# Performance work log

Hardware: AMD Instinct MI355X
Metric: run time of the kernel (lower is better)

Reference implementation:

```python
import jax, jax.numpy as jnp
import numpy as np

# Model dims (match init_kwargs)
B, S = 2, 2048
H = 1024          # hidden_size
I = 256           # intermediate_size
E = 256           # n_routed_experts
K = 8             # num_experts_per_tok
G = 8             # n_group
TG = 4            # topk_group
NS = 2            # n_shared_experts


def setup_inputs() -> dict:
    key = jax.random.key(0)
    ks = jax.random.split(key, 6)
    s = 0.02
    return {
        "x": jax.random.normal(ks[0], (B, S, H), jnp.float32),
        "Wg": jax.random.normal(ks[1], (E, H), jnp.float32) * s,          # gate Linear weight [E,H] (y = x @ Wg.T)
        "W_gate_up": jax.random.normal(ks[2], (E, H, 2 * I), jnp.float32) * s,  # per-expert gate_up proj
        "W_down": jax.random.normal(ks[3], (E, I, H), jnp.float32) * s,          # per-expert down proj
        "Ws_gate_up": jax.random.normal(ks[4], (NS, H, 2 * I), jnp.float32) * s, # shared experts
        "Ws_down": jax.random.normal(ks[5], (NS, I, H), jnp.float32) * s,
    }


def _mlp(x, w_gu, w_d):
    # DeepSeekV3 MLP: down( silu(gate) * up ); gate/up are the two chunks of gate_up
    gu = x @ w_gu                      # [N, 2I]
    g, u = gu[..., :I], gu[..., I:]
    return (jax.nn.silu(g) * u) @ w_d  # [N, H]


def reference(x, Wg, W_gate_up, W_down, Ws_gate_up, Ws_down):
    b, s, h = x.shape
    xf = x.reshape(-1, h)              # [N, H]
    n = xf.shape[0]

    # ---- shared experts (always active, averaged) ----
    shared = (_mlp(xf, Ws_gate_up[0], Ws_down[0]) + _mlp(xf, Ws_gate_up[1], Ws_down[1])) / NS

    # ---- grouped top-k gating ----
    logits = xf @ Wg.T                               # [N, E]
    gsize = E // G
    gl = logits.reshape(n, G, gsize)                 # [N, G, gsize]
    g_top_l, g_top_i = jax.lax.top_k(gl, TG)         # top-TG within each group
    cand_l = g_top_l.reshape(n, G * TG)              # candidate logits (group-major)
    cand_i = g_top_i.reshape(n, G * TG)              # within-group expert ids
    top_l, pos = jax.lax.top_k(cand_l, K)            # global top-K over candidates
    topk_idx = (pos // TG) * gsize + jnp.take_along_axis(cand_i, pos, axis=1)  # [N, K]
    topk_w = jax.nn.softmax(top_l, axis=-1)          # [N, K]

    # ---- routed experts: sort-by-expert + grouped GEMM (ragged_dot) ----
    flat_idx = topk_idx.reshape(-1)                  # [N*K]
    flat_w = topk_w.reshape(-1)
    order = jnp.argsort(flat_idx)                    # tokens grouped by expert id
    tok = order // K                                 # source token of each assignment
    xs = xf[tok]                                     # [N*K, H] gathered tokens, expert-contiguous
    gsz = jnp.bincount(flat_idx, length=E).astype(jnp.int32)  # tokens per expert

    gu = jax.lax.ragged_dot(xs, W_gate_up, gsz)      # [N*K, 2I] grouped GEMM 1
    hmid = jax.nn.silu(gu[:, :I]) * gu[:, I:]
    yo = jax.lax.ragged_dot(hmid, W_down, gsz)       # [N*K, H] grouped GEMM 2
    yo = yo * flat_w[order][:, None]                 # weight by gate prob

    routed = jnp.zeros_like(xf).at[tok].add(yo)      # scatter-add combine

    return (shared + routed).reshape(b, s, h)
```

## Files before the change

kernel.cpp:

```cpp
#include <hip/hip_runtime.h>
#include <hip/hip_bf16.h>


typedef __attribute__((ext_vector_type(4))) float  f32x4;
typedef __attribute__((ext_vector_type(8))) short  bf16x8;
typedef __attribute__((ext_vector_type(4))) short  bf16x4;
typedef __attribute__((ext_vector_type(4))) unsigned short u16x4;

#define DI static __device__ __forceinline__

DI unsigned short f2bf(float f){
  unsigned u = __builtin_bit_cast(unsigned, f);
  return (unsigned short)((u + 0x7FFFu + ((u>>16)&1u)) >> 16);
}
DI float bf2f(unsigned short s){
  return __builtin_bit_cast(float, ((unsigned)s)<<16);
}

#define WS_XBF      0u
#define WS_HSH      8388608u
#define WS_HMID     12582912u
#define WS_YSLOT    29360128u
#define WS_WGT      29360128u
#define WS_TOPKI    96468992u
#define WS_TOPKW    96600064u
#define WS_TOKMAP   96731136u
#define WS_SLOTMAP  96862208u
#define WS_CNT      96993280u
#define WS_CURSOR   96994304u
#define WS_ZERO     96995328u
#define WS_OFF      96999424u

__global__ __launch_bounds__(256) void k_wgT(const float* __restrict__ Wg, float* __restrict__ WgT){
  __shared__ float t[64][65];
  const int tid = threadIdx.x;
  const int hx = blockIdx.x * 64;
  const int ex = blockIdx.y * 64;
  #pragma unroll
  for (int k=0;k<16;++k){
    int i = (tid>>6)*16 + k, j = tid&63;
    t[i][j] = Wg[(size_t)(ex+i)*1024 + hx + j];
  }
  __syncthreads();
  #pragma unroll
  for (int k=0;k<16;++k){
    int i = (tid>>6)*16 + k, j = tid&63;
    WgT[(size_t)(hx+i)*256 + ex + j] = t[j][i];
  }
}

__global__ __launch_bounds__(256) void k_router(const float* __restrict__ x, const float* __restrict__ WgT,
                                                unsigned short* __restrict__ xbf,
                                                int* __restrict__ topki, float* __restrict__ topkw,
                                                int* __restrict__ cnt){
  __shared__ float xs[8][1024];
  __shared__ float lg[8][256];
  __shared__ float cv[8][32];
  __shared__ int   ce[8][32];
  const int tid = threadIdx.x;
  const int t0  = blockIdx.x * 8;
  {
    const f32x4* xg = (const f32x4*)(x + (size_t)t0*1024);
    f32x4* xs4 = (f32x4*)&xs[0][0];
    u16x4* xb4 = (u16x4*)(xbf + (size_t)t0*1024);
    #pragma unroll
    for (int i=0;i<8;++i){
      f32x4 v = xg[tid + i*256];
      xs4[tid + i*256] = v;
      u16x4 p; p[0]=f2bf(v[0]); p[1]=f2bf(v[1]); p[2]=f2bf(v[2]); p[3]=f2bf(v[3]);
      xb4[tid + i*256] = p;
    }
  }
  __syncthreads();
  {
    f32x4 a4[8];
    #pragma unroll
    for (int t=0;t<8;++t) a4[t] = (f32x4){0.f,0.f,0.f,0.f};
    const float* wc = WgT + tid;
    for (int h4=0; h4<256; ++h4){
      float w0 = wc[(size_t)(h4*4+0)*256];
      float w1 = wc[(size_t)(h4*4+1)*256];
      float w2 = wc[(size_t)(h4*4+2)*256];
      float w3 = wc[(size_t)(h4*4+3)*256];
      f32x4 wv = (f32x4){w0,w1,w2,w3};
      #pragma unroll
      for (int t=0;t<8;++t){
        f32x4 xv = *((const f32x4*)&xs[t][0] + h4);
        a4[t] += wv * xv;
      }
    }
    #pragma unroll
    for (int t=0;t<8;++t){
      double d = ((double)a4[t][0] + (double)a4[t][1]) + ((double)a4[t][2] + (double)a4[t][3]);
      lg[t][tid] = (float)d;
    }
  }
  __syncthreads();
  if (tid < 64){
    int tok = tid>>3, grp = tid&7;
    unsigned mask = 0;
    for (int j=0;j<4;++j){
      float best = -3.4e38f; int bi = 0;
      for (int i=0;i<32;++i){
        float v = lg[tok][grp*32+i];
        if (!((mask>>i)&1u) && v > best){ best=v; bi=i; }
      }
      mask |= 1u<<bi;
      cv[tok][grp*4+j] = best; ce[tok][grp*4+j] = grp*32+bi;
    }
  }
  __syncthreads();
  if (tid < 8){
    int tok = tid; unsigned mask=0;
    float vals[8]; int es[8];
    #pragma unroll
    for (int k=0;k<8;++k){
      float best=-3.4e38f; int bp=0;
      for (int p=0;p<32;++p){
        float v = cv[tok][p];
        if (!((mask>>p)&1u) && v > best){ best=v; bp=p; }
      }
      mask|=1u<<bp; vals[k]=best; es[k]=ce[tok][bp];
    }
    float m = vals[0], s=0.f, w[8];
    #pragma unroll
    for (int k=0;k<8;++k){ w[k]=expf(vals[k]-m); s+=w[k]; }
    float inv = 1.f/s;
    #pragma unroll
    for (int k=0;k<8;++k){
      int g=(t0+tok)*8+k;
      topki[g]=es[k]; topkw[g]=w[k]*inv;
      atomicAdd(&cnt[es[k]],1);
    }
  }
}

__global__ void k_scan(const int* __restrict__ cnt, int* __restrict__ off){
  __shared__ int s[256];
  int tid=threadIdx.x;
  s[tid]=cnt[tid]; __syncthreads();
  for (int d=1; d<256; d<<=1){
    int v = (tid>=d)? s[tid-d] : 0; __syncthreads();
    s[tid]+=v; __syncthreads();
  }
  off[tid+1]=s[tid]; if(tid==0) off[0]=0;
}

__global__ void k_scatter(const int* __restrict__ topki, const int* __restrict__ off,
                          int* __restrict__ cursor, int* __restrict__ tokmap, int* __restrict__ slotmap){
  int g = blockIdx.x*256 + threadIdx.x;
  int e = topki[g];
  int p = off[e] + atomicAdd(&cursor[e], 1);
  tokmap[p] = g >> 3;
  slotmap[g] = p;
}

template<int GEMM>
__global__ __launch_bounds__(512, 4) void k_gemm(
    const unsigned short* __restrict__ A1, const unsigned short* __restrict__ A2,
    const float* __restrict__ WE, const float* __restrict__ WS,
    const int* __restrict__ cnt, const int* __restrict__ off,
    const int* __restrict__ tokmap,
    unsigned short* __restrict__ O1, unsigned short* __restrict__ O2,
    float* __restrict__ OD, const unsigned short* __restrict__ zpage)
{
  __shared__ __align__(16) char smem[65536];
  const int bx = blockIdx.x, mt = blockIdx.y, nc = blockIdx.z;
  const bool sh = (bx >= 256);
  int e = bx, s = 0, M, Moff;
  if (!sh){ M = cnt[e]; Moff = mt*256; }
  else {
    int sidx = bx - 256;
    if (GEMM==1){ s = sidx>>3; Moff = (sidx&7)*512 + mt*256; }
    else        { s = 0;       Moff = sidx*1024 + mt*256; }
    M = 4096;
  }
  if (Moff >= M) return;
  const int tid=threadIdx.x, ln=tid&63, wv=tid>>6, wm=wv>>2, wn=wv&3, lrow=ln&15, lk=ln>>4;
  const int Ktot = (GEMM==1)?1024:(sh?512:256);
  const int ldB  = (GEMM==1)?512:1024;
  const float* Bp = (GEMM==1) ? (sh? WS + (size_t)s*524288 : WE + (size_t)e*524288)
                              : (sh? WS : WE + (size_t)e*262144);
  const int offe = sh? 0 : off[e];

  const char* a_src[2];
  #pragma unroll
  for (int qi=0;qi<2;++qi){
    int row  = (wv*2+qi)*16 + (ln>>2);
    int grow = Moff + row;
    const unsigned short* p;
    if (GEMM==1){
      if (!sh) p = (grow < M)? A1 + (size_t)tokmap[offe+grow]*1024 : zpage;
      else     p = A1 + (size_t)grow*1024;
    } else {
      if (!sh) p = (grow < M)? A1 + ((size_t)offe+grow)*256 : zpage;
      else     p = A2 + (size_t)grow*512;
    }
    a_src[qi] = (const char*)p + (ln&3)*16;
  }
  const char* b_src[2];
  {
    int swz = ((wv>>1)&3)<<2;
    int cg  = (ln&31) ^ swz;
    int c4  = cg*4;
    int gcol = (GEMM==1) ? ((c4<64)? nc*64 + c4 : 256 + nc*64 + (c4-64))
                         : (nc*128 + c4);
    int rbase = 4*wv + (ln>>5);
    #pragma unroll
    for (int q=0;q<2;++q)
      b_src[q] = (const char*)(Bp + (size_t)(rbase + 2*q)*ldB + gcol);
  }

  f32x4 acc[8][2] = {};

  auto stage = [&](int buf, int k0){
    #pragma unroll
    for (int qi=0;qi<2;++qi)
      __builtin_amdgcn_global_load_lds((const void*)(a_src[qi] + (size_t)k0*2),
          (void*)(smem + buf*16384 + (wv*2+qi)*1024), 16, 0, 0);
    #pragma unroll
    for (int q=0;q<2;++q)
      __builtin_amdgcn_global_load_lds((const void*)(b_src[q] + (size_t)k0*ldB*4),
          (void*)(smem + 32768 + buf*16384 + wv*2048 + q*1024), 16, 0, 0);
  };

  auto compute = [&](int buf){
    const short* as  = (const short*)(smem + buf*16384);
    const float* bs  = (const float*)(smem + 32768 + buf*16384);
    bf16x8 bv[2];
    #pragma unroll
    for (int ni=0;ni<2;++ni){
      int tc = (GEMM==1)? (ni*64 + wn*16 + lrow) : (wn*32 + ni*16 + lrow);
      int sloff = ((((tc>>2) ^ (lk<<2))<<2) | (tc&3));
      const float* colp = bs + (size_t)lk*8*128 + sloff;
      #pragma unroll
      for (int j=0;j<8;++j){
        unsigned u = __builtin_bit_cast(unsigned, colp[(size_t)j*128]);
        bv[ni][j] = (short)((u + 0x8000u) >> 16);
      }
    }
    #pragma unroll
    for (int mi=0;mi<8;++mi){
      bf16x8 af = *(const bf16x8*)(as + (wm*128+mi*16+lrow)*32 + lk*8);
      acc[mi][0] = __builtin_amdgcn_mfma_f32_16x16x32_bf16(af, bv[0], acc[mi][0], 0,0,0);
      acc[mi][1] = __builtin_amdgcn_mfma_f32_16x16x32_bf16(af, bv[1], acc[mi][1], 0,0,0);
    }
  };

  stage(0, 0);
  const int ns = Ktot>>5;
  for (int t=0;t<ns;++t){
    int b = t&1;
    if (t+1<ns){
      stage(b^1, (t+1)<<5);
      asm volatile("s_waitcnt vmcnt(4)" ::: "memory");
    } else {
      asm volatile("s_waitcnt vmcnt(0)" ::: "memory");
    }
    asm volatile("s_barrier" ::: "memory");
    compute(b);
    asm volatile("s_barrier" ::: "memory");
  }

  if (GEMM==1){
    __syncthreads();
    unsigned short* Hs = (unsigned short*)smem;
    #pragma unroll
    for (int mi=0;mi<8;++mi){
      f32x4 g = acc[mi][0], u = acc[mi][1];
      #pragma unroll
      for (int r=0;r<4;++r){
        float gg = g[r];
        float hh = (gg / (1.f + __expf(-gg))) * u[r];
        int m = wm*128 + mi*16 + lk*4 + r;
        Hs[m*72 + wn*16 + lrow] = f2bf(hh);
      }
    }
    __syncthreads();
    #pragma unroll
    for (int i=0;i<4;++i){
      int id = tid + i*512, m = id>>3, c8 = id&7;
      int grow = Moff + m;
      if (grow < M){
        unsigned short* dst = (!sh) ? O1 + ((size_t)offe + grow)*256 + nc*64 + c8*8
                                    : O2 + (size_t)grow*512 + (size_t)s*256 + nc*64 + c8*8;
        *(f32x4*)dst = *(const f32x4*)(Hs + m*72 + c8*8);
      }
    }
  } else {
    if (sh){
      #pragma unroll
      for (int mi=0;mi<8;++mi)
        #pragma unroll
        for (int ni=0;ni<2;++ni)
          #pragma unroll
          for (int r=0;r<4;++r){
            int m = Moff + wm*128 + mi*16 + lk*4 + r;
            int c = nc*128 + wn*32 + ni*16 + lrow;
            OD[(size_t)m*1024 + c] = acc[mi][ni][r]*0.5f;
          }
    } else {
      __syncthreads();
      unsigned short* Hs = (unsigned short*)smem;
      #pragma unroll
      for (int mi=0;mi<8;++mi)
        #pragma unroll
        for (int ni=0;ni<2;++ni)
          #pragma unroll
          for (int r=0;r<4;++r){
            int m = wm*128 + mi*16 + lk*4 + r;
            int c = wn*32 + ni*16 + lrow;
            Hs[m*128 + c] = f2bf(acc[mi][ni][r]);
          }
      __syncthreads();
      #pragma unroll
      for (int i=0;i<8;++i){
        int id = tid + i*512, m = id>>4, c8 = id&15;
        int grow = Moff + m;
        if (grow < M){
          unsigned short* dst = O1 + ((size_t)offe+grow)*1024 + nc*128 + c8*8;
          *(f32x4*)dst = *(const f32x4*)(Hs + m*128 + c8*8);
        }
      }
    }
  }
}

__global__ void k_final(float* __restrict__ out, const unsigned short* __restrict__ yslot,
                        const int* __restrict__ slotmap, const float* __restrict__ topkw){
  __shared__ int sp[8]; __shared__ float sw[8];
  int t = blockIdx.x, tid = threadIdx.x;
  if (tid<8){ sp[tid]=slotmap[t*8+tid]; sw[tid]=topkw[t*8+tid]; }
  __syncthreads();
  int c = tid*4;
  f32x4 o = *(f32x4*)(out + (size_t)t*1024 + c);
  #pragma unroll
  for (int k=0;k<8;++k){
    u16x4 y = *(const u16x4*)(yslot + (size_t)sp[k]*1024 + c);
    float w = sw[k];
    o[0] += w*bf2f(y[0]); o[1] += w*bf2f(y[1]); o[2] += w*bf2f(y[2]); o[3] += w*bf2f(y[3]);
  }
  *(f32x4*)(out + (size_t)t*1024 + c) = o;
}

extern "C" void kernel_launch(void* const* d_in, const int* in_sizes, int n_in,
                              void* d_out, int out_size, void* d_ws, size_t ws_size,
                              hipStream_t stream) {
  const float* x    = (const float*)d_in[0];
  const float* Wg   = (const float*)d_in[1];
  const float* Wgu  = (const float*)d_in[2];
  const float* Wd   = (const float*)d_in[3];
  const float* Wsgu = (const float*)d_in[4];
  const float* Wsd  = (const float*)d_in[5];
  float* out = (float*)d_out;

  char* W = (char*)d_ws;
  unsigned short* xbf    = (unsigned short*)(W + WS_XBF);
  unsigned short* hsh    = (unsigned short*)(W + WS_HSH);
  unsigned short* hmid   = (unsigned short*)(W + WS_HMID);
  unsigned short* yslot  = (unsigned short*)(W + WS_YSLOT);
  float* WgT     = (float*)(W + WS_WGT);
  int*   topki   = (int*)(W + WS_TOPKI);
  float* topkw   = (float*)(W + WS_TOPKW);
  int*   tokmap  = (int*)(W + WS_TOKMAP);
  int*   slotmap = (int*)(W + WS_SLOTMAP);
  int*   cnt     = (int*)(W + WS_CNT);
  int*   cursor  = (int*)(W + WS_CURSOR);
  unsigned short* zpage = (unsigned short*)(W + WS_ZERO);
  int*   off     = (int*)(W + WS_OFF);

  hipMemsetAsync((void*)cnt, 0, 1024+1024+4096, stream);

  k_wgT    <<<dim3(16,4), 256, 0, stream>>>(Wg, WgT);
  k_router <<<512, 256, 0, stream>>>(x, WgT, xbf, topki, topkw, cnt);
  k_scan   <<<1, 256, 0, stream>>>(cnt, off);
  k_scatter<<<128, 256, 0, stream>>>(topki, off, cursor, tokmap, slotmap);
  k_gemm<1><<<dim3(272,2,4), 512, 0, stream>>>(xbf, (const unsigned short*)nullptr,
        Wgu, Wsgu, cnt, off, tokmap, hmid, hsh, out, zpage);
  k_gemm<2><<<dim3(260,4,8), 512, 0, stream>>>(hmid, hsh,
        Wd, Wsd, cnt, off, tokmap, yslot, (unsigned short*)nullptr, out, zpage);
  k_final <<<4096, 256, 0, stream>>>(out, yslot, slotmap, topkw);
}
```

Before: 352.4 us.

## Stage B weights through registers as bf16 to shrink LDS footprint

```diff
diff --git a/kernel.cpp b/kernel.cpp
--- a/kernel.cpp
+++ b/kernel.cpp
@@ -164,7 +164,7 @@
     unsigned short* __restrict__ O1, unsigned short* __restrict__ O2,
     float* __restrict__ OD, const unsigned short* __restrict__ zpage)
 {
-  __shared__ __align__(16) char smem[65536];
+  __shared__ __align__(16) char smem[49152];
   const int bx = blockIdx.x, mt = blockIdx.y, nc = blockIdx.z;
   const bool sh = (bx >= 256);
   int e = bx, s = 0, M, Moff;
@@ -198,46 +198,50 @@
     }
     a_src[qi] = (const char*)p + (ln&3)*16;
   }
-  const char* b_src[2];
-  {
-    int swz = ((wv>>1)&3)<<2;
-    int cg  = (ln&31) ^ swz;
-    int c4  = cg*4;
-    int gcol = (GEMM==1) ? ((c4<64)? nc*64 + c4 : 256 + nc*64 + (c4-64))
-                         : (nc*128 + c4);
-    int rbase = 4*wv + (ln>>5);
-    #pragma unroll
-    for (int q=0;q<2;++q)
-      b_src[q] = (const char*)(Bp + (size_t)(rbase + 2*q)*ldB + gcol);
-  }
+  const int b_kk = 4*wv + (ln>>4);
+  const int b_c0 = (ln&15)*8;
+  const float* b_base[2];
+  #pragma unroll
+  for (int q=0;q<2;++q){
+    int c = b_c0 + 4*q;
+    int gcol = (GEMM==1)? ((c<64)? nc*64 + c : 256 + nc*64 + (c-64)) : (nc*128 + c);
+    b_base[q] = Bp + (size_t)b_kk*ldB + gcol;
+  }
+  const int b_wcol = b_c0 ^ ((wv>>1)<<3);
 
   f32x4 acc[8][2] = {};
-
-  auto stage = [&](int buf, int k0){
+  f32x4 brg0[2], brg1[2];
+
+  auto stageA = [&](int buf, int k0){
     #pragma unroll
     for (int qi=0;qi<2;++qi)
       __builtin_amdgcn_global_load_lds((const void*)(a_src[qi] + (size_t)k0*2),
           (void*)(smem + buf*16384 + (wv*2+qi)*1024), 16, 0, 0);
+  };
+  auto loadB = [&](f32x4* brg, int k0){
     #pragma unroll
     for (int q=0;q<2;++q)
-      __builtin_amdgcn_global_load_lds((const void*)(b_src[q] + (size_t)k0*ldB*4),
-          (void*)(smem + 32768 + buf*16384 + wv*2048 + q*1024), 16, 0, 0);
+      brg[q] = *(const f32x4*)(b_base[q] + (size_t)k0*ldB);
   };
-
+  auto writeB = [&](const f32x4* brg, int buf){
+    bf16x8 v;
+    #pragma unroll
+    for (int q=0;q<2;++q)
+      #pragma unroll
+      for (int j=0;j<4;++j)
+        v[q*4+j] = (short)f2bf(brg[q][j]);
+    *(bf16x8*)(smem + 32768 + buf*8192 + (b_kk*128 + b_wcol)*2) = v;
+  };
   auto compute = [&](int buf){
-    const short* as  = (const short*)(smem + buf*16384);
-    const float* bs  = (const float*)(smem + 32768 + buf*16384);
+    const short* as = (const short*)(smem + buf*16384);
+    const short* bs = (const short*)(smem + 32768 + buf*8192);
     bf16x8 bv[2];
     #pragma unroll
     for (int ni=0;ni<2;++ni){
       int tc = (GEMM==1)? (ni*64 + wn*16 + lrow) : (wn*32 + ni*16 + lrow);
-      int sloff = ((((tc>>2) ^ (lk<<2))<<2) | (tc&3));
-      const float* colp = bs + (size_t)lk*8*128 + sloff;
-      #pragma unroll
-      for (int j=0;j<8;++j){
-        unsigned u = __builtin_bit_cast(unsigned, colp[(size_t)j*128]);
-        bv[ni][j] = (short)((u + 0x8000u) >> 16);
-      }
+      const short* p = bs + lk*8*128 + (tc ^ (lk<<3));
+      #pragma unroll
+      for (int j=0;j<8;++j) bv[ni][j] = p[j*128];
     }
     #pragma unroll
     for (int mi=0;mi<8;++mi){
@@ -247,18 +251,33 @@
     }
   };
 
-  stage(0, 0);
   const int ns = Ktot>>5;
-  for (int t=0;t<ns;++t){
-    int b = t&1;
+  loadB(brg0, 0);
+  stageA(0, 0);
+  loadB(brg1, 32);
+  asm volatile("s_waitcnt vmcnt(2)" ::: "memory");
+  writeB(brg0, 0);
+  asm volatile("s_waitcnt lgkmcnt(0)" ::: "memory");
+  asm volatile("s_barrier" ::: "memory");
+  for (int t=0; t<ns; t+=2){
+    if (t+1<ns) stageA(1, (t+1)<<5);
+    compute(0);
     if (t+1<ns){
-      stage(b^1, (t+1)<<5);
-      asm volatile("s_waitcnt vmcnt(4)" ::: "memory");
-    } else {
       asm volatile("s_waitcnt vmcnt(0)" ::: "memory");
+      writeB(brg1, 1);
+      if (t+2<ns) loadB(brg0, (t+2)<<5);
+      asm volatile("s_waitcnt lgkmcnt(0)" ::: "memory");
     }
     asm volatile("s_barrier" ::: "memory");
-    compute(b);
+    if (t+1>=ns) break;
+    if (t+2<ns) stageA(0, (t+2)<<5);
+    compute(1);
+    if (t+2<ns){
+      asm volatile("s_waitcnt vmcnt(0)" ::: "memory");
+      writeB(brg0, 0);
+      if (t+3<ns) loadB(brg1, (t+3)<<5);
+      asm volatile("s_waitcnt lgkmcnt(0)" ::: "memory");
+    }
     asm volatile("s_barrier" ::: "memory");
   }
 
@@ -300,26 +319,31 @@
             OD[(size_t)m*1024 + c] = acc[mi][ni][r]*0.5f;
           }
     } else {
-      __syncthreads();
       unsigned short* Hs = (unsigned short*)smem;
       #pragma unroll
-      for (int mi=0;mi<8;++mi)
+      for (int pass=0; pass<2; ++pass){
+        __syncthreads();
+        if ((wn>>1) == pass){
+          #pragma unroll
+          for (int mi=0;mi<8;++mi)
+            #pragma unroll
+            for (int ni=0;ni<2;++ni)
+              #pragma unroll
+              for (int r=0;r<4;++r){
+                int m = wm*128 + mi*16 + lk*4 + r;
+                int c = (wn&1)*32 + ni*16 + lrow;
+                Hs[m*72 + c] = f2bf(acc[mi][ni][r]);
+              }
+        }
+        __syncthreads();
         #pragma unroll
-        for (int ni=0;ni<2;++ni)
-          #pragma unroll
-          for (int r=0;r<4;++r){
-            int m = wm*128 + mi*16 + lk*4 + r;
-            int c = wn*32 + ni*16 + lrow;
-            Hs[m*128 + c] = f2bf(acc[mi][ni][r]);
+        for (int i=0;i<4;++i){
+          int id = tid + i*512, m = id>>3, c8 = id&7;
+          int grow = Moff + m;
+          if (grow < M){
+            unsigned short* dst = O1 + ((size_t)offe+grow)*1024 + nc*128 + pass*64 + c8*8;
+            *(f32x4*)dst = *(const f32x4*)(Hs + m*72 + c8*8);
           }
-      __syncthreads();
-      #pragma unroll
-      for (int i=0;i<8;++i){
-        int id = tid + i*512, m = id>>4, c8 = id&15;
-        int grow = Moff + m;
-        if (grow < M){
-          unsigned short* dst = O1 + ((size_t)offe+grow)*1024 + nc*128 + c8*8;
-          *(f32x4*)dst = *(const f32x4*)(Hs + m*128 + c8*8);
         }
       }
     }
```

Result: slower. 377.2 us (+7.0%).

## Fuse weighted scatter-add combine into down-proj GEMM epilogue via atomics

Applied to the files above, without the earlier changes.

```diff
diff --git a/kernel.cpp b/kernel.cpp
--- a/kernel.cpp
+++ b/kernel.cpp
@@ -20,12 +20,11 @@
 #define WS_XBF      0u
 #define WS_HSH      8388608u
 #define WS_HMID     12582912u
-#define WS_YSLOT    29360128u
 #define WS_WGT      29360128u
 #define WS_TOPKI    96468992u
 #define WS_TOPKW    96600064u
 #define WS_TOKMAP   96731136u
-#define WS_SLOTMAP  96862208u
+#define WS_WMAP     96862208u
 #define WS_CNT      96993280u
 #define WS_CURSOR   96994304u
 #define WS_ZERO     96995328u
@@ -146,13 +145,14 @@
   off[tid+1]=s[tid]; if(tid==0) off[0]=0;
 }
 
-__global__ void k_scatter(const int* __restrict__ topki, const int* __restrict__ off,
-                          int* __restrict__ cursor, int* __restrict__ tokmap, int* __restrict__ slotmap){
+__global__ void k_scatter(const int* __restrict__ topki, const float* __restrict__ topkw,
+                          const int* __restrict__ off, int* __restrict__ cursor,
+                          int* __restrict__ tokmap, float* __restrict__ wmap){
   int g = blockIdx.x*256 + threadIdx.x;
   int e = topki[g];
   int p = off[e] + atomicAdd(&cursor[e], 1);
   tokmap[p] = g >> 3;
-  slotmap[g] = p;
+  wmap[p]   = topkw[g];
 }
 
 template<int GEMM>
@@ -160,7 +160,7 @@
     const unsigned short* __restrict__ A1, const unsigned short* __restrict__ A2,
     const float* __restrict__ WE, const float* __restrict__ WS,
     const int* __restrict__ cnt, const int* __restrict__ off,
-    const int* __restrict__ tokmap,
+    const int* __restrict__ tokmap, const float* __restrict__ wmap,
     unsigned short* __restrict__ O1, unsigned short* __restrict__ O2,
     float* __restrict__ OD, const unsigned short* __restrict__ zpage)
 {
@@ -297,50 +297,31 @@
           for (int r=0;r<4;++r){
             int m = Moff + wm*128 + mi*16 + lk*4 + r;
             int c = nc*128 + wn*32 + ni*16 + lrow;
-            OD[(size_t)m*1024 + c] = acc[mi][ni][r]*0.5f;
+            atomicAdd(&OD[(size_t)m*1024 + c], acc[mi][ni][r]*0.5f);
           }
     } else {
       __syncthreads();
-      unsigned short* Hs = (unsigned short*)smem;
+      int*   stok = (int*)smem;
+      float* swgt = (float*)(smem + 1024);
+      if (tid < 256){
+        int gr = Moff + tid;
+        if (gr < M){ stok[tid] = tokmap[offe+gr]; swgt[tid] = wmap[offe+gr]; }
+      }
+      __syncthreads();
       #pragma unroll
       for (int mi=0;mi<8;++mi)
         #pragma unroll
         for (int ni=0;ni<2;++ni)
           #pragma unroll
           for (int r=0;r<4;++r){
-            int m = wm*128 + mi*16 + lk*4 + r;
-            int c = wn*32 + ni*16 + lrow;
-            Hs[m*128 + c] = f2bf(acc[mi][ni][r]);
+            int lr = wm*128 + mi*16 + lk*4 + r;
+            if (Moff + lr < M){
+              int c = nc*128 + wn*32 + ni*16 + lrow;
+              atomicAdd(&OD[(size_t)stok[lr]*1024 + c], swgt[lr]*acc[mi][ni][r]);
+            }
           }
-      __syncthreads();
-      #pragma unroll
-      for (int i=0;i<8;++i){
-        int id = tid + i*512, m = id>>4, c8 = id&15;
-        int grow = Moff + m;
-        if (grow < M){
-          unsigned short* dst = O1 + ((size_t)offe+grow)*1024 + nc*128 + c8*8;
-          *(f32x4*)dst = *(const f32x4*)(Hs + m*128 + c8*8);
-        }
-      }
-    }
-  }
-}
-
-__global__ void k_final(float* __restrict__ out, const unsigned short* __restrict__ yslot,
-                        const int* __restrict__ slotmap, const float* __restrict__ topkw){
-  __shared__ int sp[8]; __shared__ float sw[8];
-  int t = blockIdx.x, tid = threadIdx.x;
-  if (tid<8){ sp[tid]=slotmap[t*8+tid]; sw[tid]=topkw[t*8+tid]; }
-  __syncthreads();
-  int c = tid*4;
-  f32x4 o = *(f32x4*)(out + (size_t)t*1024 + c);
-  #pragma unroll
-  for (int k=0;k<8;++k){
-    u16x4 y = *(const u16x4*)(yslot + (size_t)sp[k]*1024 + c);
-    float w = sw[k];
-    o[0] += w*bf2f(y[0]); o[1] += w*bf2f(y[1]); o[2] += w*bf2f(y[2]); o[3] += w*bf2f(y[3]);
-  }
-  *(f32x4*)(out + (size_t)t*1024 + c) = o;
+    }
+  }
 }
 
 extern "C" void kernel_launch(void* const* d_in, const int* in_sizes, int n_in,
@@ -358,26 +339,25 @@
   unsigned short* xbf    = (unsigned short*)(W + WS_XBF);
   unsigned short* hsh    = (unsigned short*)(W + WS_HSH);
   unsigned short* hmid   = (unsigned short*)(W + WS_HMID);
-  unsigned short* yslot  = (unsigned short*)(W + WS_YSLOT);
   float* WgT     = (float*)(W + WS_WGT);
   int*   topki   = (int*)(W + WS_TOPKI);
   float* topkw   = (float*)(W + WS_TOPKW);
   int*   tokmap  = (int*)(W + WS_TOKMAP);
-  int*   slotmap = (int*)(W + WS_SLOTMAP);
+  float* wmap    = (float*)(W + WS_WMAP);
   int*   cnt     = (int*)(W + WS_CNT);
   int*   cursor  = (int*)(W + WS_CURSOR);
   unsigned short* zpage = (unsigned short*)(W + WS_ZERO);
   int*   off     = (int*)(W + WS_OFF);
 
   hipMemsetAsync((void*)cnt, 0, 1024+1024+4096, stream);
+  hipMemsetAsync((void*)out, 0, (size_t)out_size*4, stream);
 
   k_wgT    <<<dim3(16,4), 256, 0, stream>>>(Wg, WgT);
   k_router <<<512, 256, 0, stream>>>(x, WgT, xbf, topki, topkw, cnt);
   k_scan   <<<1, 256, 0, stream>>>(cnt, off);
-  k_scatter<<<128, 256, 0, stream>>>(topki, off, cursor, tokmap, slotmap);
+  k_scatter<<<128, 256, 0, stream>>>(topki, topkw, off, cursor, tokmap, wmap);
   k_gemm<1><<<dim3(272,2,4), 512, 0, stream>>>(xbf, (const unsigned short*)nullptr,
-        Wgu, Wsgu, cnt, off, tokmap, hmid, hsh, out, zpage);
+        Wgu, Wsgu, cnt, off, tokmap, wmap, hmid, hsh, out, zpage);
   k_gemm<2><<<dim3(260,4,8), 512, 0, stream>>>(hmid, hsh,
-        Wd, Wsd, cnt, off, tokmap, yslot, (unsigned short*)nullptr, out, zpage);
-  k_final <<<4096, 256, 0, stream>>>(out, yslot, slotmap, topkw);
-}
+        Wd, Wsd, cnt, off, tokmap, wmap, (unsigned short*)nullptr, (unsigned short*)nullptr, out, zpage);
+}
```

After: 394.5 us. 11.9% more time.
